# Optimization experiments

Hardware: AMD Instinct MI355X
Metric: run time of the kernel (lower is better)

The kernel has to match this reference:

```python
import jax, jax.numpy as jnp
import numpy as np

N = 100000      # nodes
E = 1600000     # edges (before self-loops)
IN = 128        # in_channels
HID = 16        # hidden per head
HEADS = 8
OUT = 16        # out_channels (classes)
NEG_SLOPE = 0.2


def setup_inputs() -> dict:
    key = jax.random.key(0)
    ks = jax.random.split(key, 10)
    x = jax.random.normal(ks[0], (N, IN), jnp.float32)
    edge_index = jax.random.randint(ks[1], (2, E), 0, N, jnp.int32)
    g = lambda k, shape, fan: (jax.random.normal(k, shape, jnp.float32)
                               * (1.0 / np.sqrt(fan)).astype(np.float32))
    # layer 1: in -> heads*hid
    W1 = g(ks[2], (IN, HEADS * HID), IN)
    att_src1 = g(ks[3], (HEADS, HID), HID)
    att_dst1 = g(ks[4], (HEADS, HID), HID)
    b1 = jnp.zeros((HEADS * HID,), jnp.float32)
    # layer 2: heads*hid -> out, 1 head, concat=False
    W2 = g(ks[5], (HEADS * HID, OUT), HEADS * HID)
    att_src2 = g(ks[6], (1, OUT), OUT)
    att_dst2 = g(ks[7], (1, OUT), OUT)
    b2 = jnp.zeros((OUT,), jnp.float32)
    return dict(x=x, edge_index=edge_index, W1=W1, att_src1=att_src1,
                att_dst1=att_dst1, b1=b1, W2=W2, att_src2=att_src2,
                att_dst2=att_dst2, b2=b2)


def gat_conv(x, src, dst, W, a_src, a_dst, b, concat):
    """PyG-style GATConv (eval mode). src->dst message flow."""
    num_nodes = x.shape[0]
    H, C = a_src.shape
    h = (x @ W).reshape(num_nodes, H, C)                      # [N,H,C]
    # per-node attention halves, gathered to edges
    e = (h * a_src).sum(-1)[src] + (h * a_dst).sum(-1)[dst]   # [Etot,H]
    e = jax.nn.leaky_relu(e, NEG_SLOPE)
    # segment softmax over edges grouped by destination node
    emax = jax.ops.segment_max(e, dst, num_segments=num_nodes)    # [N,H]
    ee = jnp.exp(e - emax[dst])
    denom = jax.ops.segment_sum(ee, dst, num_segments=num_nodes)  # [N,H]
    alpha = ee / (denom[dst] + 1e-16)                              # [Etot,H]
    # weighted scatter-aggregate of source features
    msg = h[src] * alpha[:, :, None]                               # [Etot,H,C]
    out = jax.ops.segment_sum(msg, dst, num_segments=num_nodes)    # [N,H,C]
    out = out.reshape(num_nodes, H * C) if concat else out.mean(axis=1)
    return out + b


def reference(x, edge_index, W1, att_src1, att_dst1, b1,
              W2, att_src2, att_dst2, b2):
    # add self loops (PyG GATConv default)
    loop = jnp.arange(N, dtype=edge_index.dtype)
    src = jnp.concatenate([edge_index[0], loop])
    dst = jnp.concatenate([edge_index[1], loop])

    h = gat_conv(x, src, dst, W1, att_src1, att_dst1, b1, concat=True)
    embeddings = jax.nn.elu(h)
    logits = gat_conv(embeddings, src, dst, W2, att_src2, att_dst2, b2,
                      concat=False)
    return jax.nn.log_softmax(logits, axis=1), embeddings
```

## Files before the change

### kernel.cpp

```cpp
#include <hip/hip_runtime.h>
#include <hip/hip_bf16.h>
#include <math.h>

#define N_NODES 100000
#define E_EDGES 1600000
#define ETOT    (E_EDGES + N_NODES)
#define NEG     0.2f

#define SH        8
#define NBUCK     ((N_NODES + 255) >> 8)
#define BIN_TILE  4096
#define NBIN      ((E_EDGES + BIN_TILE - 1) / BIN_TILE)
#define CAP_B     5120

#define NMFMA     ((N_NODES + 63) / 64)
#define G_A       782
#define G_B       (NMFMA - G_A)

typedef __attribute__((ext_vector_type(8))) short bf16x8;
typedef __attribute__((ext_vector_type(4))) float f32x4;
typedef __attribute__((ext_vector_type(2))) short bf16p;

__device__ inline float lrelu(float x) { return x > 0.f ? x : NEG * x; }
__device__ inline float bflo(unsigned int b) { return __uint_as_float(b << 16); }
__device__ inline float bfhi(unsigned int b) { return __uint_as_float(b & 0xFFFF0000u); }
__device__ inline unsigned short f2bf(float f) {
    unsigned int u = __float_as_uint(f);
    return (unsigned short)((u + 0x7FFFu + ((u >> 16) & 1u)) >> 16);
}

__device__ inline float dot2bf(unsigned int wp, unsigned int hp, float c) {
#if __has_builtin(__builtin_amdgcn_fdot2_f32_bf16)
    return __builtin_amdgcn_fdot2_f32_bf16(__builtin_bit_cast(bf16p, wp),
                                           __builtin_bit_cast(bf16p, hp),
                                           c, false);
#else
    return fmaf(bflo(wp), bflo(hp), fmaf(bfhi(wp), bfhi(hp), c));
#endif
}

__device__ inline int exscan256(int v, int* wscr, int t) {
    int lane = t & 63, wid = t >> 6;
    int incl = v;
#pragma unroll
    for (int ofs = 1; ofs < 64; ofs <<= 1) {
        int u = __shfl_up(incl, ofs, 64);
        if (lane >= ofs) incl += u;
    }
    if (lane == 63) wscr[wid] = incl;
    __syncthreads();
    int wpre = 0;
#pragma unroll
    for (int w = 0; w < 4; ++w) wpre += (w < wid) ? wscr[w] : 0;
    return wpre + incl - v;
}

__global__ __launch_bounds__(256) void k_wt(const float* __restrict__ W,
                                            unsigned short* __restrict__ wtg) {
    int t = blockIdx.x * 256 + threadIdx.x;
    if (t >= 128 * 128) return;
    int n = t >> 7, k = t & 127;
    wtg[t] = f2bf(W[k * 128 + n]);
}

__device__ __forceinline__ void gemm1_role(
    int n0, int t, unsigned short (*xb)[136],
    const float* __restrict__ x, const unsigned short* __restrict__ wtg,
    const float* __restrict__ asrc, const float* __restrict__ adst,
    __hip_bfloat16* __restrict__ h1b, unsigned short* __restrict__ s1b,
    float* __restrict__ d1) {
#pragma unroll
    for (int i = 0; i < 8; ++i) {
        int i4 = t + i * 256;
        int r = i4 >> 5;
        int c = (i4 & 31) * 4;
        float4 v = make_float4(0.f, 0.f, 0.f, 0.f);
        if (n0 + r < N_NODES) v = *(const float4*)(x + (size_t)(n0 + r) * 128 + c);
        xb[r][c + 0] = f2bf(v.x);
        xb[r][c + 1] = f2bf(v.y);
        xb[r][c + 2] = f2bf(v.z);
        xb[r][c + 3] = f2bf(v.w);
    }
    __syncthreads();

    int l = t & 63, wv = t >> 6;
    int col = l & 15, q4 = l >> 4;
    int rbase = wv * 16;
    int koff = q4 * 8;

    bf16x8 a[4];
#pragma unroll
    for (int st = 0; st < 4; ++st)
        a[st] = *(const bf16x8*)&xb[rbase + col][st * 32 + koff];

    int nodeb = n0 + rbase + q4 * 4;
#pragma unroll
    for (int nt = 0; nt < 8; ++nt) {
        f32x4 acc = {0.f, 0.f, 0.f, 0.f};
        const unsigned short* wrow = wtg + (size_t)(nt * 16 + col) * 128 + koff;
#pragma unroll
        for (int st = 0; st < 4; ++st) {
            bf16x8 b = *(const bf16x8*)(wrow + st * 32);
            acc = __builtin_amdgcn_mfma_f32_16x16x32_bf16(a[st], b, acc, 0, 0, 0);
        }
        float as_v = asrc[nt * 16 + col];
        float ad_v = adst[nt * 16 + col];
#pragma unroll
        for (int r = 0; r < 4; ++r) {
            int node = nodeb + r;
            if (node < N_NODES)
                h1b[(size_t)node * 128 + nt * 16 + col] = __float2bfloat16(acc[r]);
            float ps = acc[r] * as_v, pd = acc[r] * ad_v;
#pragma unroll
            for (int ofs = 1; ofs < 16; ofs <<= 1) {
                ps += __shfl_xor(ps, ofs, 64);
                pd += __shfl_xor(pd, ofs, 64);
            }
            if (col == 0 && node < N_NODES) {
                s1b[node * 8 + nt] = f2bf(ps);
                d1[node * 8 + nt] = pd;
            }
        }
    }
}

union SmemBin {
    struct {
        int2 st[BIN_TILE];
        int  hist[NBUCK + 1];
        int  lstart[NBUCK];
        int  gbase[NBUCK];
        int  wscr[4];
    } b;
    unsigned short xb[64][136];
};

__global__ __launch_bounds__(256) void k_parBin(
    const int* __restrict__ src, const int* __restrict__ dst,
    int* __restrict__ gcur, int2* __restrict__ coo,
    const float* __restrict__ x, const unsigned short* __restrict__ wtg,
    const float* __restrict__ asrc, const float* __restrict__ adst,
    __hip_bfloat16* __restrict__ h1b, unsigned short* __restrict__ s1b,
    float* __restrict__ d1) {
    __shared__ SmemBin sm;
    int bid = blockIdx.x, t = threadIdx.x;
    bool isBin = (bid % 3 == 0) && (bid / 3 < NBIN);
    if (!isBin) {
        int gid = bid - bid / 3 - 1;
        gemm1_role(gid * 64, t, sm.xb, x, wtg, asrc, adst, h1b, s1b, d1);
        return;
    }
    int wb = bid / 3;
    int e0 = wb * BIN_TILE;
    int nE = min(BIN_TILE, E_EDGES - e0);
    for (int i = t; i <= NBUCK; i += 256) sm.b.hist[i] = 0;
    __syncthreads();
    for (int i = t; i < nE; i += 256)
        atomicAdd(&sm.b.hist[dst[e0 + i] >> SH], 1);
    __syncthreads();
    int i0 = 2 * t, i1 = 2 * t + 1;
    int h0 = (i0 < NBUCK) ? sm.b.hist[i0] : 0;
    int h1v = (i1 < NBUCK) ? sm.b.hist[i1] : 0;
    int s = h0 + h1v;
    int pre = exscan256(s, sm.b.wscr, t);
    __syncthreads();
    if (i0 < NBUCK) sm.b.hist[i0] = pre;
    if (i1 < NBUCK) sm.b.hist[i1] = pre + h0;
    if (t == 255) sm.b.hist[NBUCK] = pre + s;
    __syncthreads();
    for (int i = t; i < NBUCK; i += 256) {
        int st_ = sm.b.hist[i];
        int cnt = sm.b.hist[i + 1] - st_;
        sm.b.lstart[i] = st_;
        if (cnt > 0) sm.b.gbase[i] = i * CAP_B + atomicAdd(&gcur[i], cnt);
    }
    __syncthreads();
    for (int i = t; i < nE; i += 256) {
        int sv = src[e0 + i], dv = dst[e0 + i];
        int p = atomicAdd(&sm.b.hist[dv >> SH], 1);
        sm.b.st[p] = make_int2(sv, dv);
    }
    __syncthreads();
    for (int i = t; i < nE; i += 256) {
        int2 e = sm.b.st[i];
        int b2 = e.y >> SH;
        int slot = sm.b.gbase[b2] + (i - sm.b.lstart[b2]);
        slot = min(slot, (b2 + 1) * CAP_B - 1);
        coo[slot] = e;
    }
}

__global__ __launch_bounds__(256) void k_scanb(const int* __restrict__ gcur,
                                               int* __restrict__ bbase,
                                               int* __restrict__ off) {
    __shared__ int wscr[4];
    int t = threadIdx.x;
    int i0 = 2 * t, i1 = 2 * t + 1;
    int a = 0, b = 0;
    if (i0 < NBUCK) a = min(gcur[i0], CAP_B) + min(256, N_NODES - (i0 << SH));
    if (i1 < NBUCK) b = min(gcur[i1], CAP_B) + min(256, N_NODES - (i1 << SH));
    int s = a + b;
    int pre = exscan256(s, wscr, t);
    if (i0 < NBUCK) bbase[i0] = pre;
    if (i1 < NBUCK) bbase[i1] = pre + a;
    if (t == 0) off[N_NODES] = ETOT;
}

union SmemFine {
    struct {
        int ldeg[256];
        int lsrc[CAP_B + 256];
        int wscr[4];
    } f;
    unsigned short xb[64][136];
};

__global__ __launch_bounds__(256) void k_parFine(
    const int2* __restrict__ coo, const int* __restrict__ gcur,
    const int* __restrict__ bbase, int* __restrict__ off,
    int* __restrict__ csr,
    const float* __restrict__ x, const unsigned short* __restrict__ wtg,
    const float* __restrict__ asrc, const float* __restrict__ adst,
    __hip_bfloat16* __restrict__ h1b, unsigned short* __restrict__ s1b,
    float* __restrict__ d1) {
    __shared__ SmemFine sm;
    int bid = blockIdx.x, t = threadIdx.x;
    bool isFine = (bid % 3 == 0) && (bid / 3 < NBUCK);
    if (!isFine) {
        int gid = bid - bid / 3 - 1;
        gemm1_role((G_A + gid) * 64, t, sm.xb, x, wtg, asrc, adst,
                   h1b, s1b, d1);
        return;
    }
    int b = bid / 3;
    int n0 = b << SH;
    int nn = min(256, N_NODES - n0);
    int ecnt = min(gcur[b], CAP_B);
    int base = bbase[b];
    const int2* seg = coo + (size_t)b * CAP_B;

    sm.f.ldeg[t] = 0;
    __syncthreads();
    for (int i = t; i < ecnt; i += 256)
        atomicAdd(&sm.f.ldeg[seg[i].y - n0], 1);
    __syncthreads();
    int d = (t < nn) ? sm.f.ldeg[t] + 1 : 0;
    int myoff = exscan256(d, sm.f.wscr, t);
    __syncthreads();
    if (t < nn) {
        off[n0 + t] = base + myoff;
        sm.f.lsrc[myoff] = n0 + t;
        sm.f.ldeg[t] = myoff + 1;
    }
    __syncthreads();
    for (int i = t; i < ecnt; i += 256) {
        int2 e = seg[i];
        int p = atomicAdd(&sm.f.ldeg[e.y - n0], 1);
        sm.f.lsrc[p] = e.x;
    }
    __syncthreads();
    int tot = ecnt + nn;
    for (int i = t; i < tot; i += 256)
        csr[base + i] = sm.f.lsrc[i];
}

__global__ __launch_bounds__(256) void k_l1(
    const int* __restrict__ off, const int* __restrict__ csr,
    const unsigned short* __restrict__ s1b, const float* __restrict__ d1,
    const uint4* __restrict__ h1q, const float* __restrict__ b1,
    float* __restrict__ emb,
    const float* __restrict__ W2, const float* __restrict__ as2,
    const float* __restrict__ ad2, unsigned short* __restrict__ h2s,
    float* __restrict__ s2, float* __restrict__ d2v) {
    __shared__ float esh[4][128];
    int t = threadIdx.x;
    int node = blockIdx.x * 4 + (t >> 6);
    int wv = t >> 6;
    int l = t & 63;
    int g = l >> 4, q = l & 15;
    int hb = q >> 1;
    int lo = off[node], hi = off[node + 1];
    float dvh = d1[node * 8 + hb];

    float acc[8];
#pragma unroll
    for (int c = 0; c < 8; ++c) acc[c] = 0.f;
    float den = 0.f;

    int idx = lo + g;
    bool have = (idx + 4 < hi);
    int sa = 0, sb = 0;
    uint4 ba = make_uint4(0, 0, 0, 0), bb = make_uint4(0, 0, 0, 0);
    float sva = 0.f, svb = 0.f;
    if (have) {
        sa = csr[idx]; sb = csr[idx + 4];
        ba = h1q[(size_t)sa * 16 + q];
        bb = h1q[(size_t)sb * 16 + q];
        sva = __uint_as_float((unsigned)s1b[(size_t)sa * 8 + hb] << 16);
        svb = __uint_as_float((unsigned)s1b[(size_t)sb * 8 + hb] << 16);
    }
    while (have) {
        int nidx = idx + 8;
        bool nhave = (nidx + 4 < hi);
        int na = 0, nb = 0;
        uint4 nba = make_uint4(0, 0, 0, 0), nbb = make_uint4(0, 0, 0, 0);
        float nsa = 0.f, nsb = 0.f;
        if (nhave) {
            na = csr[nidx]; nb = csr[nidx + 4];
            nba = h1q[(size_t)na * 16 + q];
            nbb = h1q[(size_t)nb * 16 + q];
            nsa = __uint_as_float((unsigned)s1b[(size_t)na * 8 + hb] << 16);
            nsb = __uint_as_float((unsigned)s1b[(size_t)nb * 8 + hb] << 16);
        }
        float w0 = __expf(lrelu(sva + dvh));
        float w1 = __expf(lrelu(svb + dvh));
        den += w0 + w1;
        unsigned int wp;
        asm("v_cvt_pk_bf16_f32 %0, %1, %2" : "=v"(wp) : "v"(w0), "v"(w1));
        unsigned int p0, p1;
        p0 = __builtin_amdgcn_perm(bb.x, ba.x, 0x05040100u);
        p1 = __builtin_amdgcn_perm(bb.x, ba.x, 0x07060302u);
        acc[0] = dot2bf(wp, p0, acc[0]);
        acc[1] = dot2bf(wp, p1, acc[1]);
        p0 = __builtin_amdgcn_perm(bb.y, ba.y, 0x05040100u);
        p1 = __builtin_amdgcn_perm(bb.y, ba.y, 0x07060302u);
        acc[2] = dot2bf(wp, p0, acc[2]);
        acc[3] = dot2bf(wp, p1, acc[3]);
        p0 = __builtin_amdgcn_perm(bb.z, ba.z, 0x05040100u);
        p1 = __builtin_amdgcn_perm(bb.z, ba.z, 0x07060302u);
        acc[4] = dot2bf(wp, p0, acc[4]);
        acc[5] = dot2bf(wp, p1, acc[5]);
        p0 = __builtin_amdgcn_perm(bb.w, ba.w, 0x05040100u);
        p1 = __builtin_amdgcn_perm(bb.w, ba.w, 0x07060302u);
        acc[6] = dot2bf(wp, p0, acc[6]);
        acc[7] = dot2bf(wp, p1, acc[7]);
        sa = na; sb = nb; ba = nba; bb = nbb; sva = nsa; svb = nsb;
        idx = nidx; have = nhave;
    }
    if (idx < hi) {
        int sc = csr[idx];
        uint4 bv = h1q[(size_t)sc * 16 + q];
        float sv = __uint_as_float((unsigned)s1b[(size_t)sc * 8 + hb] << 16);
        float w = __expf(lrelu(sv + dvh));
        den += w;
        acc[0] = fmaf(w, bflo(bv.x), acc[0]);
        acc[1] = fmaf(w, bfhi(bv.x), acc[1]);
        acc[2] = fmaf(w, bflo(bv.y), acc[2]);
        acc[3] = fmaf(w, bfhi(bv.y), acc[3]);
        acc[4] = fmaf(w, bflo(bv.z), acc[4]);
        acc[5] = fmaf(w, bfhi(bv.z), acc[5]);
        acc[6] = fmaf(w, bflo(bv.w), acc[6]);
        acc[7] = fmaf(w, bfhi(bv.w), acc[7]);
    }
#pragma unroll
    for (int c = 0; c < 8; ++c) {
        acc[c] += __shfl_xor(acc[c], 16, 64);
        acc[c] += __shfl_xor(acc[c], 32, 64);
    }
    den += __shfl_xor(den, 16, 64);
    den += __shfl_xor(den, 32, 64);

    if (l < 16) {
        float r = 1.f / den;
        float vv[8];
#pragma unroll
        for (int c = 0; c < 8; ++c) {
            float v = acc[c] * r + b1[8 * q + c];
            vv[c] = v > 0.f ? v : expm1f(v);
            esh[wv][8 * q + c] = vv[c];
        }
        float4* ep = (float4*)(emb + (size_t)node * 128);
        ep[2 * q]     = make_float4(vv[0], vv[1], vv[2], vv[3]);
        ep[2 * q + 1] = make_float4(vv[4], vv[5], vv[6], vv[7]);
    }
    __syncthreads();

    int j = l & 15, part = l >> 4;
    float o = 0.f;
#pragma unroll
    for (int cc = 0; cc < 32; ++cc) {
        int c = 4 * cc + part;
        o = fmaf(esh[wv][c], W2[c * 16 + j], o);
    }
    o += __shfl_xor(o, 16, 64);
    o += __shfl_xor(o, 32, 64);
    float ps = o * as2[j], pd = o * ad2[j];
#pragma unroll
    for (int ofs = 1; ofs < 16; ofs <<= 1) {
        ps += __shfl_xor(ps, ofs, 16);
        pd += __shfl_xor(pd, ofs, 16);
    }
    if (l < 16) h2s[(size_t)node * 16 + j] = f2bf(o);
    if (l == 0) { s2[node] = ps; d2v[node] = pd; }
}

__global__ __launch_bounds__(256) void k_l2(
    const int* __restrict__ off, const int* __restrict__ csr,
    const float* __restrict__ s2, const float* __restrict__ d2,
    const unsigned int* __restrict__ h2w, const float* __restrict__ b2,
    float* __restrict__ logits) {
    int t = threadIdx.x;
    int node = blockIdx.x * 4 + (t >> 6);
    int l = t & 63;
    int g = l >> 3, p = l & 7;
    int lo = off[node], hi = off[node + 1];
    float dv = d2[node];

    float ax = 0.f, ay = 0.f, den = 0.f;
    int idx = lo + g;
    int him = hi - 1;
    if (idx + 8 < hi) {
        int s0 = csr[idx], s1i = csr[idx + 8];
        unsigned int pa = h2w[(size_t)s0 * 8 + p];
        unsigned int pb = h2w[(size_t)s1i * 8 + p];
        float wa = s2[s0], wb = s2[s1i];
        int ia = csr[min(idx + 16, him)];
        int ib = csr[min(idx + 24, him)];
        while (true) {
            unsigned int npa = h2w[(size_t)ia * 8 + p];
            unsigned int npb = h2w[(size_t)ib * 8 + p];
            float nwa = s2[ia], nwb = s2[ib];
            int nia = csr[min(idx + 32, him)];
            int nib = csr[min(idx + 40, him)];
            float w0 = __expf(lrelu(wa + dv));
            float w1 = __expf(lrelu(wb + dv));
            den += w0 + w1;
            unsigned int wp;
            asm("v_cvt_pk_bf16_f32 %0, %1, %2" : "=v"(wp) : "v"(w0), "v"(w1));
            unsigned int p0 = __builtin_amdgcn_perm(pb, pa, 0x05040100u);
            unsigned int p1 = __builtin_amdgcn_perm(pb, pa, 0x07060302u);
            ax = dot2bf(wp, p0, ax);
            ay = dot2bf(wp, p1, ay);
            idx += 16;
            if (idx + 8 >= hi) break;
            pa = npa; pb = npb; wa = nwa; wb = nwb;
            ia = nia; ib = nib;
        }
    }
    if (idx < hi) {
        int s = csr[idx];
        float w = __expf(lrelu(s2[s] + dv));
        den += w;
        unsigned int bv = h2w[(size_t)s * 8 + p];
        ax = fmaf(w, bflo(bv), ax);
        ay = fmaf(w, bfhi(bv), ay);
    }
#pragma unroll
    for (int ofs = 8; ofs < 64; ofs <<= 1) {
        ax += __shfl_xor(ax, ofs, 64);
        ay += __shfl_xor(ay, ofs, 64);
        den += __shfl_xor(den, ofs, 64);
    }
    float r = 1.f / den;
    float v0 = ax * r + b2[2 * p], v1 = ay * r + b2[2 * p + 1];
    float mm = fmaxf(v0, v1);
#pragma unroll
    for (int ofs = 1; ofs < 8; ofs <<= 1) mm = fmaxf(mm, __shfl_xor(mm, ofs, 8));
    float sm = __expf(v0 - mm) + __expf(v1 - mm);
#pragma unroll
    for (int ofs = 1; ofs < 8; ofs <<= 1) sm += __shfl_xor(sm, ofs, 8);
    if (g == 0) {
        float ls = logf(sm);
        logits[node * 16 + 2 * p]     = v0 - mm - ls;
        logits[node * 16 + 2 * p + 1] = v1 - mm - ls;
    }
}

extern "C" void kernel_launch(void* const* d_in, const int* in_sizes, int n_in,
                              void* d_out, int out_size, void* d_ws, size_t ws_size,
                              hipStream_t stream) {
    const float* x   = (const float*)d_in[0];
    const int*   ei  = (const int*)d_in[1];
    const float* W1  = (const float*)d_in[2];
    const float* as1 = (const float*)d_in[3];
    const float* ad1 = (const float*)d_in[4];
    const float* b1  = (const float*)d_in[5];
    const float* W2  = (const float*)d_in[6];
    const float* as2 = (const float*)d_in[7];
    const float* ad2 = (const float*)d_in[8];
    const float* b2  = (const float*)d_in[9];

    float* out    = (float*)d_out;
    float* logits = out;
    float* emb    = out + (size_t)N_NODES * 16;

    float* ws    = (float*)d_ws;
    unsigned int* h1w = (unsigned int*)ws;
    int2*  coo   = (int2*)(h1w + (size_t)N_NODES * 64);
    unsigned short* s1b = (unsigned short*)(coo + (size_t)NBUCK * CAP_B);
    float* d1    = (float*)(s1b + (size_t)N_NODES * 8);
    unsigned short* h2s = (unsigned short*)(d1 + (size_t)N_NODES * 8);
    float* s2    = (float*)(h2s + (size_t)N_NODES * 16);
    float* d2v   = s2 + (size_t)N_NODES;
    int*   offs  = (int*)(d2v + (size_t)N_NODES);
    int*   csr   = offs + N_NODES + 2;
    int*   gcur  = csr + ETOT;
    int*   bbase = gcur + NBUCK;
    unsigned short* wtg = (unsigned short*)(bbase + NBUCK);

    const int* srcp = ei;
    const int* dstp = ei + E_EDGES;

    hipMemsetAsync(gcur, 0, (size_t)NBUCK * sizeof(int), stream);

    k_wt<<<64, 256, 0, stream>>>(W1, wtg);
    k_parBin<<<NBIN + G_A, 256, 0, stream>>>(srcp, dstp, gcur, coo,
                                             x, wtg, as1, ad1,
                                             (__hip_bfloat16*)h1w, s1b, d1);
    k_scanb<<<1, 256, 0, stream>>>(gcur, bbase, offs);
    k_parFine<<<NBUCK + G_B, 256, 0, stream>>>(coo, gcur, bbase, offs, csr,
                                               x, wtg, as1, ad1,
                                               (__hip_bfloat16*)h1w, s1b, d1);

    k_l1<<<N_NODES / 4, 256, 0, stream>>>(offs, csr, s1b, d1,
                                          (const uint4*)h1w, b1, emb,
                                          W2, as2, ad2, h2s, s2, d2v);

    k_l2<<<N_NODES / 4, 256, 0, stream>>>(offs, csr, s2, d2v,
                                          (const unsigned int*)h2s, b2, logits);
}
```

Baseline: 245.4 us.

## Sort nodes by in-degree before aggregation kernels to balance wavefront work

```diff
diff --git a/kernel.cpp b/kernel.cpp
--- a/kernel.cpp
+++ b/kernel.cpp
@@ -12,10 +12,12 @@
 #define BIN_TILE  4096
 #define NBIN      ((E_EDGES + BIN_TILE - 1) / BIN_TILE)
 #define CAP_B     5120
+#define DBINS     64
 
 #define NMFMA     ((N_NODES + 63) / 64)
 #define G_A       782
 #define G_B       (NMFMA - G_A)
+#define NODE_BLK  ((N_NODES + 255) / 256)
 
 typedef __attribute__((ext_vector_type(8))) short bf16x8;
 typedef __attribute__((ext_vector_type(4))) float f32x4;
@@ -264,7 +266,55 @@
         csr[base + i] = sm.f.lsrc[i];
 }
 
+__global__ __launch_bounds__(256) void k_dcnt(const int* __restrict__ off,
+                                              int* __restrict__ dhist) {
+    __shared__ int lh[DBINS];
+    int t = threadIdx.x;
+    int n = blockIdx.x * 256 + t;
+    if (t < DBINS) lh[t] = 0;
+    __syncthreads();
+    if (n < N_NODES) {
+        int bin = min(off[n + 1] - off[n], DBINS - 1);
+        atomicAdd(&lh[bin], 1);
+    }
+    __syncthreads();
+    if (t < DBINS && lh[t] > 0) atomicAdd(&dhist[t], lh[t]);
+}
+
+__global__ void k_dbase(const int* __restrict__ dhist, int* __restrict__ dcur) {
+    int t = threadIdx.x;
+    int v = dhist[t];
+    int incl = v;
+#pragma unroll
+    for (int ofs = 1; ofs < 64; ofs <<= 1) {
+        int u = __shfl_up(incl, ofs, 64);
+        if (t >= ofs) incl += u;
+    }
+    dcur[t] = incl - v;
+}
+
+__global__ __launch_bounds__(256) void k_dscat(const int* __restrict__ off,
+                                               int* __restrict__ dcur,
+                                               int* __restrict__ perm) {
+    __shared__ int lh[DBINS], lbase[DBINS];
+    int t = threadIdx.x;
+    int n = blockIdx.x * 256 + t;
+    if (t < DBINS) lh[t] = 0;
+    __syncthreads();
+    int bin = 0, lr = 0;
+    bool valid = (n < N_NODES);
+    if (valid) {
+        bin = min(off[n + 1] - off[n], DBINS - 1);
+        lr = atomicAdd(&lh[bin], 1);
+    }
+    __syncthreads();
+    if (t < DBINS && lh[t] > 0) lbase[t] = atomicAdd(&dcur[t], lh[t]);
+    __syncthreads();
+    if (valid) perm[lbase[bin] + lr] = n;
+}
+
 __global__ __launch_bounds__(256) void k_l1(
+    const int* __restrict__ perm,
     const int* __restrict__ off, const int* __restrict__ csr,
     const unsigned short* __restrict__ s1b, const float* __restrict__ d1,
     const uint4* __restrict__ h1q, const float* __restrict__ b1,
@@ -274,7 +324,7 @@
     float* __restrict__ s2, float* __restrict__ d2v) {
     __shared__ float esh[4][128];
     int t = threadIdx.x;
-    int node = blockIdx.x * 4 + (t >> 6);
+    int node = perm[(blockIdx.x << 2) + (t >> 6)];
     int wv = t >> 6;
     int l = t & 63;
     int g = l >> 4, q = l & 15;
@@ -395,12 +445,13 @@
 }
 
 __global__ __launch_bounds__(256) void k_l2(
+    const int* __restrict__ perm,
     const int* __restrict__ off, const int* __restrict__ csr,
     const float* __restrict__ s2, const float* __restrict__ d2,
     const unsigned int* __restrict__ h2w, const float* __restrict__ b2,
     float* __restrict__ logits) {
     int t = threadIdx.x;
-    int node = blockIdx.x * 4 + (t >> 6);
+    int node = perm[(blockIdx.x << 2) + (t >> 6)];
     int l = t & 63;
     int g = l >> 3, p = l & 7;
     int lo = off[node], hi = off[node + 1];
@@ -495,13 +546,16 @@
     int*   offs  = (int*)(d2v + (size_t)N_NODES);
     int*   csr   = offs + N_NODES + 2;
     int*   gcur  = csr + ETOT;
-    int*   bbase = gcur + NBUCK;
-    unsigned short* wtg = (unsigned short*)(bbase + NBUCK);
+    int*   dhist = gcur + NBUCK;
+    int*   bbase = dhist + DBINS;
+    int*   dcur  = bbase + NBUCK;
+    int*   perm  = dcur + DBINS;
+    unsigned short* wtg = (unsigned short*)(perm + N_NODES);
 
     const int* srcp = ei;
     const int* dstp = ei + E_EDGES;
 
-    hipMemsetAsync(gcur, 0, (size_t)NBUCK * sizeof(int), stream);
+    hipMemsetAsync(gcur, 0, (size_t)(NBUCK + DBINS) * sizeof(int), stream);
 
     k_wt<<<64, 256, 0, stream>>>(W1, wtg);
     k_parBin<<<NBIN + G_A, 256, 0, stream>>>(srcp, dstp, gcur, coo,
@@ -512,10 +566,14 @@
                                                x, wtg, as1, ad1,
                                                (__hip_bfloat16*)h1w, s1b, d1);
 
-    k_l1<<<N_NODES / 4, 256, 0, stream>>>(offs, csr, s1b, d1,
+    k_dcnt<<<NODE_BLK, 256, 0, stream>>>(offs, dhist);
+    k_dbase<<<1, 64, 0, stream>>>(dhist, dcur);
+    k_dscat<<<NODE_BLK, 256, 0, stream>>>(offs, dcur, perm);
+
+    k_l1<<<N_NODES / 4, 256, 0, stream>>>(perm, offs, csr, s1b, d1,
                                           (const uint4*)h1w, b1, emb,
                                           W2, as2, ad2, h2s, s2, d2v);
 
-    k_l2<<<N_NODES / 4, 256, 0, stream>>>(offs, csr, s2, d2v,
+    k_l2<<<N_NODES / 4, 256, 0, stream>>>(perm, offs, csr, s2, d2v,
                                           (const unsigned int*)h2s, b2, logits);
 }
```

Result: slower. 260.3 us (+6.1%).
